# Performance work log

Measured on AMD Instinct MI355X. Metric: run time of the kernel, lower is better.

Reference implementation:

```python
import jax, jax.numpy as jnp
import numpy as np

B, S, D, H = 4, 1024, 512, 8
EPS = 1e-5


def _cx(x):
    # [..., 2] float -> complex
    return jax.lax.complex(x[..., 0], x[..., 1])


def setup_inputs() -> dict:
    key = jax.random.key(0)
    ks = jax.random.split(key, 9)
    f = lambda k, sh: jax.random.normal(k, sh, dtype=jnp.float32)
    inp = {
        "q": f(ks[0], (B, S, D, 2)),
        "k": f(ks[1], (B, S, D, 2)),
        "v": f(ks[2], (B, S, D, 2)),
        "Wq": f(ks[3], (D, D, 2)) * 0.02,
        "bq": f(ks[4], (D, 2)) * 0.02,
        "Wk": f(ks[5], (D, D, 2)) * 0.02,
        "bk": f(ks[6], (D, 2)) * 0.02,
        "Wv": f(ks[7], (D, D, 2)) * 0.02,
        "bv": f(ks[8], (D, 2)) * 0.02,
        "gamma_r": jnp.ones((D,), jnp.float32),
        "beta_r": jnp.zeros((D,), jnp.float32),
        "gamma_i": jnp.ones((D,), jnp.float32),
        "beta_i": jnp.zeros((D,), jnp.float32),
        "n_heads": H,
    }
    return inp


def _layernorm(x, g, b):
    # torch LayerNorm: biased variance, eps inside sqrt
    mu = jnp.mean(x, axis=-1, keepdims=True)
    var = jnp.mean((x - mu) ** 2, axis=-1, keepdims=True)
    return (x - mu) / jnp.sqrt(var + EPS) * g + b


def reference(q, k, v, Wq, bq, Wk, bk, Wv, bv, gamma_r, beta_r, gamma_i, beta_i, n_heads):
    qc, kc, vc = _cx(q), _cx(k), _cx(v)
    # complex linear: x @ W^T + b
    Q = jnp.einsum("bsd,ed->bse", qc, _cx(Wq)) + _cx(bq)
    K = jnp.einsum("bsd,ed->bse", kc, _cx(Wk)) + _cx(bk)
    V = jnp.einsum("bsd,ed->bse", vc, _cx(Wv)) + _cx(bv)
    b, s, d = qc.shape
    dh = d // n_heads
    Qh = Q.reshape(b, s, n_heads, dh)
    Kh = K.reshape(b, s, n_heads, dh)
    Vh = V.reshape(b, s, n_heads, dh)
    # complex scores [b,h,q,k], scaled by sqrt(dh)
    scores = jnp.einsum("bqhd,bkhd->bhqk", Qh, Kh) / jnp.sqrt(jnp.float32(dh))
    # original: softmax over view_as_real dim=-2 == key axis, real & imag independently
    attn = jax.lax.complex(jax.nn.softmax(scores.real, axis=-1),
                           jax.nn.softmax(scores.imag, axis=-1))
    # (dropout is identity in eval mode)
    out = jnp.einsum("bhqk,bkhd->bqhd", attn, Vh).reshape(b, s, d)
    out = out + qc  # residual
    out_r = _layernorm(out.real, gamma_r, beta_r)
    out_i = _layernorm(out.imag, gamma_i, beta_i)
    return jnp.stack([out_r, out_i], axis=-1)  # [B,S,D,2]
```

## Files before the change

### kernel.cpp

```cpp
#include <hip/hip_runtime.h>
#include <math.h>

#define BB  4
#define SS  1024
#define DD  512
#define HH  8
#define DHD 64
#define PL  2097152
#define WPL 262144

constexpr float LN_EPS = 1e-5f;

using half4 = __attribute__((ext_vector_type(4))) _Float16;
using half8 = __attribute__((ext_vector_type(8))) _Float16;
using f32x4 = __attribute__((ext_vector_type(4))) float;

__device__ __forceinline__ half8 negh(half8 a) {
    union { half8 h; unsigned int u[4]; } t;
    t.h = a;
    #pragma unroll
    for (int i = 0; i < 4; ++i) t.u[i] ^= 0x80008000u;
    return t.h;
}
__device__ __forceinline__ half8 ldh64(const unsigned short* p, int row, int col) {
    return *(const half8*)(p + row * 64 + (col ^ ((row & 7) << 3)));
}
#define MFMA16(acc, a, b) acc = __builtin_amdgcn_mfma_f32_16x16x32_f16(a, b, acc, 0, 0, 0)

__global__ __launch_bounds__(256)
void cvt_kernel(const float2* __restrict__ s0, const float2* __restrict__ s1,
                const float2* __restrict__ s2, unsigned short* __restrict__ dst,
                int planeElems) {
    const int z = blockIdx.y;
    const float2* src = z == 0 ? s0 : (z == 1 ? s1 : s2);
    unsigned short* base = dst + (size_t)z * 2 * planeElems;
    const int idx = (blockIdx.x * 256 + threadIdx.x) * 2;
    float4 t = *(const float4*)(src + idx);
    const int m = idx >> 9;
    const int d = idx & 511;
    const int ob = (((m >> 7) << 3) + (d >> 6)) * 8192 + ((m & 127) << 6) + (d & 63);
    union { _Float16 h[2]; unsigned int u; } r, i;
    r.h[0] = (_Float16)t.x; r.h[1] = (_Float16)t.z;
    i.h[0] = (_Float16)t.y; i.h[1] = (_Float16)t.w;
    *(unsigned int*)(base + ob) = r.u;
    *(unsigned int*)(base + planeElems + ob) = i.u;
}

__global__ __launch_bounds__(256, 2)
void proj_kernel(const unsigned short* __restrict__ XP,
                 const unsigned short* __restrict__ WP,
                 const float2* __restrict__ bq, const float2* __restrict__ bk,
                 const float2* __restrict__ bv,
                 unsigned short* __restrict__ QG, unsigned short* __restrict__ KG,
                 unsigned short* __restrict__ VG) {
    const unsigned short* XR = XP + (size_t)blockIdx.z * 2 * PL;
    const unsigned short* XI = XR + PL;
    const unsigned short* WRp = WP + (size_t)blockIdx.z * 2 * WPL;
    const unsigned short* WIp = WRp + WPL;
    const float2* bias; unsigned short* outP;
    if (blockIdx.z == 0)      { bias = bq; outP = QG; }
    else if (blockIdx.z == 1) { bias = bk; outP = KG; }
    else                      { bias = bv; outP = VG; }
    const bool isV = (blockIdx.z == 2);

    __shared__ __align__(16) unsigned short Xs[2][128 * 64];
    __shared__ __align__(16) unsigned short Ws[2][128 * 64];

    const int tid  = threadIdx.x;
    const int w    = tid >> 6;
    const int lane = tid & 63;
    const int quad = lane >> 4;
    const int l15  = lane & 15;
    const int wm   = w >> 1;
    const int we   = w & 1;
    const int m0   = blockIdx.x * 128;
    const int e0   = blockIdx.y * 128;

    const int srow = lane >> 3;
    const int sg   = lane & 7;
    const unsigned short* gplane;
    unsigned short* lb;
    int row0;
    if (w == 0)      { gplane = XR;  row0 = m0; lb = &Xs[0][0]; }
    else if (w == 1) { gplane = XI;  row0 = m0; lb = &Xs[1][0]; }
    else if (w == 2) { gplane = WRp; row0 = e0; lb = &Ws[0][0]; }
    else             { gplane = WIp; row0 = e0; lb = &Ws[1][0]; }
    const unsigned short* gs = gplane + (size_t)row0 * DD + srow * 64 + ((sg ^ srow) << 3);

    f32x4 Sr[4][4], Si[4][4];
    #pragma unroll
    for (int a = 0; a < 4; ++a)
        #pragma unroll
        for (int c = 0; c < 4; ++c) { Sr[a][c] = (f32x4)0.f; Si[a][c] = (f32x4)0.f; }

    for (int s = 0; s < 8; ++s) {
        if (s) __syncthreads();
        const unsigned short* _g = gs + (size_t)s * 8192;
        #pragma unroll
        for (int j = 0; j < 16; ++j)
            __builtin_amdgcn_global_load_lds(
                (const __attribute__((address_space(1))) void*)(_g + j * 512),
                (__attribute__((address_space(3))) void*)(lb + j * 512),
                16, 0, 0);
        __syncthreads();

        #pragma unroll
        for (int kc = 0; kc < 2; ++kc) {
            const int dl = kc * 32 + quad * 8;
            half8 xr[4], xi[4];
            #pragma unroll
            for (int mf = 0; mf < 4; ++mf) {
                const int mr = wm * 64 + mf * 16 + l15;
                xr[mf] = ldh64(Xs[0], mr, dl);
                xi[mf] = ldh64(Xs[1], mr, dl);
            }
            #pragma unroll
            for (int ef = 0; ef < 4; ++ef) {
                const int er = we * 64 + ef * 16 + l15;
                half8 wr  = ldh64(Ws[0], er, dl);
                half8 wi  = ldh64(Ws[1], er, dl);
                half8 wmi = negh(wi);
                #pragma unroll
                for (int mf = 0; mf < 4; ++mf) {
                    MFMA16(Sr[mf][ef], xr[mf], wr);
                    MFMA16(Sr[mf][ef], xi[mf], wmi);
                    MFMA16(Si[mf][ef], xr[mf], wi);
                    MFMA16(Si[mf][ef], xi[mf], wr);
                }
            }
        }
    }

    #pragma unroll
    for (int ef = 0; ef < 4; ++ef) {
        const int eg  = e0 + we * 64 + ef * 16 + l15;
        const int hh  = eg >> 6;
        const int col = eg & 63;
        float2 bb = bias[eg];
        #pragma unroll
        for (int mf = 0; mf < 4; ++mf) {
            #pragma unroll
            for (int reg = 0; reg < 4; ++reg) {
                int m = m0 + wm * 64 + mf * 16 + quad * 4 + reg;
                int bidx = m >> 10;
                int sidx = m & 1023;
                int bh = bidx * HH + hh;
                union { _Float16 h; unsigned short u; } cr, ci;
                cr.h = (_Float16)(Sr[mf][ef][reg] + bb.x);
                ci.h = (_Float16)(Si[mf][ef][reg] + bb.y);
                size_t o = isV ? ((size_t)bh * DHD + col) * SS + sidx
                               : ((size_t)bh * SS + sidx) * DHD + col;
                outP[0 * PL + o] = cr.u;
                outP[1 * PL + o] = ci.u;
            }
        }
    }
}

#define AWID 72
__global__ __launch_bounds__(256, 2)
void attn_kernel(const unsigned short* __restrict__ QG, const unsigned short* __restrict__ KG,
                 const unsigned short* __restrict__ VG,
                 unsigned short* __restrict__ ObR, unsigned short* __restrict__ ObI) {
    __shared__ unsigned short Ks[2][64 * AWID];
    __shared__ unsigned short Vt[2][64 * AWID];
    __shared__ unsigned short Ps[2][64 * AWID];
    __shared__ float lbuf[2][2][64];

    const int n   = blockIdx.x;
    const int bh  = (n & 7) * 4 + (n >> 7);
    const int q0  = ((n >> 3) & 15) * 64;
    const int b   = bh >> 3;
    const int h   = bh & 7;

    const int tid  = threadIdx.x;
    const int w    = tid >> 6;
    const int lane = tid & 63;
    const int quad = lane >> 4;
    const int l15  = lane & 15;
    const int sw   = w & 1;
    const int tw   = w >> 1;

    half8 qfr[2][2], qfi[2][2], qfmi[2][2];
    #pragma unroll
    for (int qt = 0; qt < 2; ++qt)
        #pragma unroll
        for (int kc = 0; kc < 2; ++kc) {
            size_t qa = ((size_t)bh * SS + q0 + sw * 32 + qt * 16 + l15) * DHD + kc * 32 + quad * 8;
            qfr[qt][kc]  = *(const half8*)(QG + qa);
            qfi[qt][kc]  = *(const half8*)(QG + PL + qa);
            qfmi[qt][kc] = negh(qfi[qt][kc]);
        }

    f32x4 acc[2][2][4];
    #pragma unroll
    for (int qt = 0; qt < 2; ++qt)
        #pragma unroll
        for (int dt = 0; dt < 2; ++dt)
            #pragma unroll
            for (int p = 0; p < 4; ++p) acc[qt][dt][p] = (f32x4)0.f;
    float lacc[2][2] = {{0.f, 0.f}, {0.f, 0.f}};

    const int srow = tid >> 3;
    const int sg   = (tid & 7) * 8;

    for (int kt = 0; kt < SS; kt += 64) {
        __syncthreads();
        #pragma unroll
        for (int p = 0; p < 2; ++p)
            #pragma unroll
            for (int it = 0; it < 2; ++it) {
                const int r = it * 32 + srow;
                *(uint4*)&Ks[p][r * AWID + sg] =
                    *(const uint4*)(KG + (size_t)p * PL + ((size_t)bh * SS + kt + r) * DHD + sg);
                *(uint4*)&Vt[p][r * AWID + sg] =
                    *(const uint4*)(VG + (size_t)p * PL + ((size_t)bh * DHD + r) * SS + kt + sg);
            }
        __syncthreads();

        f32x4 Sr[2][2], Si[2][2];
        #pragma unroll
        for (int a = 0; a < 2; ++a)
            #pragma unroll
            for (int c = 0; c < 2; ++c) { Sr[a][c] = (f32x4)0.f; Si[a][c] = (f32x4)0.f; }
        #pragma unroll
        for (int kc = 0; kc < 2; ++kc) {
            #pragma unroll
            for (int kt2 = 0; kt2 < 2; ++kt2) {
                const int krow = tw * 32 + kt2 * 16 + l15;
                half8 akr = *(const half8*)&Ks[0][krow * AWID + kc * 32 + quad * 8];
                half8 aki = *(const half8*)&Ks[1][krow * AWID + kc * 32 + quad * 8];
                #pragma unroll
                for (int qt = 0; qt < 2; ++qt) {
                    MFMA16(Sr[kt2][qt], akr, qfr[qt][kc]);
                    MFMA16(Sr[kt2][qt], aki, qfmi[qt][kc]);
                    MFMA16(Si[kt2][qt], aki, qfr[qt][kc]);
                    MFMA16(Si[kt2][qt], akr, qfi[qt][kc]);
                }
            }
        }

        #pragma unroll
        for (int kt2 = 0; kt2 < 2; ++kt2)
            #pragma unroll
            for (int qt = 0; qt < 2; ++qt) {
                half4 pr, pi;
                float sr_ = 0.f, si_ = 0.f;
                #pragma unroll
                for (int reg = 0; reg < 4; ++reg) {
                    float er = __expf(Sr[kt2][qt][reg] * 0.125f);
                    float ei = __expf(Si[kt2][qt][reg] * 0.125f);
                    pr[reg] = (_Float16)er;
                    pi[reg] = (_Float16)ei;
                    sr_ += (float)pr[reg];
                    si_ += (float)pi[reg];
                }
                lacc[qt][0] += sr_;
                lacc[qt][1] += si_;
                const int qrow = sw * 32 + qt * 16 + l15;
                const int kcol = tw * 32 + kt2 * 16 + quad * 4;
                *(half4*)&Ps[0][qrow * AWID + kcol] = pr;
                *(half4*)&Ps[1][qrow * AWID + kcol] = pi;
            }
        __syncthreads();

        #pragma unroll
        for (int kc = 0; kc < 2; ++kc) {
            half8 ap[2][2];
            #pragma unroll
            for (int qt = 0; qt < 2; ++qt) {
                const int qrow = sw * 32 + qt * 16 + l15;
                ap[qt][0] = *(const half8*)&Ps[0][qrow * AWID + kc * 32 + quad * 8];
                ap[qt][1] = *(const half8*)&Ps[1][qrow * AWID + kc * 32 + quad * 8];
            }
            #pragma unroll
            for (int dt = 0; dt < 2; ++dt) {
                const int drow = tw * 32 + dt * 16 + l15;
                half8 bvr = *(const half8*)&Vt[0][drow * AWID + kc * 32 + quad * 8];
                half8 bvi = *(const half8*)&Vt[1][drow * AWID + kc * 32 + quad * 8];
                #pragma unroll
                for (int qt = 0; qt < 2; ++qt) {
                    MFMA16(acc[qt][dt][0], ap[qt][0], bvr);
                    MFMA16(acc[qt][dt][1], ap[qt][0], bvi);
                    MFMA16(acc[qt][dt][2], ap[qt][1], bvr);
                    MFMA16(acc[qt][dt][3], ap[qt][1], bvi);
                }
            }
        }
    }

    __syncthreads();
    #pragma unroll
    for (int qt = 0; qt < 2; ++qt)
        #pragma unroll
        for (int p = 0; p < 2; ++p) {
            float v = lacc[qt][p];
            v += __shfl_xor(v, 16);
            v += __shfl_xor(v, 32);
            if (lane < 16) lbuf[p][tw][sw * 32 + qt * 16 + lane] = v;
        }
    __syncthreads();

    #pragma unroll
    for (int qt = 0; qt < 2; ++qt)
        #pragma unroll
        for (int reg = 0; reg < 4; ++reg) {
            const int qloc = sw * 32 + qt * 16 + quad * 4 + reg;
            const float ir = 1.f / (lbuf[0][0][qloc] + lbuf[0][1][qloc]);
            const float ii = 1.f / (lbuf[1][0][qloc] + lbuf[1][1][qloc]);
            #pragma unroll
            for (int dt = 0; dt < 2; ++dt) {
                const int d = tw * 32 + dt * 16 + l15;
                union { _Float16 h; unsigned short u; } cr, ci;
                cr.h = (_Float16)(acc[qt][dt][0][reg] * ir - acc[qt][dt][3][reg] * ii);
                ci.h = (_Float16)(acc[qt][dt][1][reg] * ir + acc[qt][dt][2][reg] * ii);
                size_t o = ((size_t)b * SS + q0 + qloc) * DD + h * DHD + d;
                ObR[o] = cr.u;
                ObI[o] = ci.u;
            }
        }
}

__global__ __launch_bounds__(256)
void ln_kernel(const unsigned short* __restrict__ OrP, const unsigned short* __restrict__ OiP,
               const float2* __restrict__ Qin,
               const float* __restrict__ gr, const float* __restrict__ br,
               const float* __restrict__ gi, const float* __restrict__ bi,
               float2* __restrict__ out) {
    const int row = blockIdx.x;
    const int tid = threadIdx.x;
    const size_t base = (size_t)row * DD;
    const int e0 = 2 * tid, e1 = 2 * tid + 1;

    union { unsigned int u; _Float16 h[2]; } tr, ti;
    tr.u = *(const unsigned int*)(OrP + base + e0);
    ti.u = *(const unsigned int*)(OiP + base + e0);
    float2 r0 = Qin[base + e0];
    float2 r1 = Qin[base + e1];
    float xr0 = (float)tr.h[0] + r0.x;
    float xr1 = (float)tr.h[1] + r1.x;
    float xi0 = (float)ti.h[0] + r0.y;
    float xi1 = (float)ti.h[1] + r1.y;

    float sr = xr0 + xr1;
    float si = xi0 + xi1;
    float qr = xr0 * xr0 + xr1 * xr1;
    float qi = xi0 * xi0 + xi1 * xi1;
    #pragma unroll
    for (int off = 32; off > 0; off >>= 1) {
        sr += __shfl_down(sr, off);
        si += __shfl_down(si, off);
        qr += __shfl_down(qr, off);
        qi += __shfl_down(qi, off);
    }
    __shared__ float red[4][4];
    __shared__ float stat[4];
    int lane = tid & 63, wid = tid >> 6;
    if (lane == 0) { red[wid][0] = sr; red[wid][1] = si; red[wid][2] = qr; red[wid][3] = qi; }
    __syncthreads();
    if (tid == 0) {
        sr = red[0][0] + red[1][0] + red[2][0] + red[3][0];
        si = red[0][1] + red[1][1] + red[2][1] + red[3][1];
        qr = red[0][2] + red[1][2] + red[2][2] + red[3][2];
        qi = red[0][3] + red[1][3] + red[2][3] + red[3][3];
        float mur = sr * (1.f / DD), mui = si * (1.f / DD);
        float vr = qr * (1.f / DD) - mur * mur;
        float vi = qi * (1.f / DD) - mui * mui;
        stat[0] = mur; stat[1] = mui;
        stat[2] = rsqrtf(vr + LN_EPS); stat[3] = rsqrtf(vi + LN_EPS);
    }
    __syncthreads();
    float mur = stat[0], mui = stat[1], rsr = stat[2], rsi = stat[3];
    out[base + e0] = make_float2((xr0 - mur) * rsr * gr[e0] + br[e0],
                                 (xi0 - mui) * rsi * gi[e0] + bi[e0]);
    out[base + e1] = make_float2((xr1 - mur) * rsr * gr[e1] + br[e1],
                                 (xi1 - mui) * rsi * gi[e1] + bi[e1]);
}

extern "C" void kernel_launch(void* const* d_in, const int* in_sizes, int n_in,
                              void* d_out, int out_size, void* d_ws, size_t ws_size,
                              hipStream_t stream) {
    const float2* q  = (const float2*)d_in[0];
    const float2* k  = (const float2*)d_in[1];
    const float2* v  = (const float2*)d_in[2];
    const float2* Wq = (const float2*)d_in[3];
    const float2* bq = (const float2*)d_in[4];
    const float2* Wk = (const float2*)d_in[5];
    const float2* bk = (const float2*)d_in[6];
    const float2* Wv = (const float2*)d_in[7];
    const float2* bv = (const float2*)d_in[8];
    const float*  gr = (const float*)d_in[9];
    const float*  br = (const float*)d_in[10];
    const float*  gi = (const float*)d_in[11];
    const float*  bi = (const float*)d_in[12];

    unsigned short* XP  = (unsigned short*)d_ws;
    unsigned short* WP  = XP + (size_t)6 * PL;
    unsigned short* QG  = WP + (size_t)6 * WPL;
    unsigned short* KG  = QG + (size_t)2 * PL;
    unsigned short* VG  = KG + (size_t)2 * PL;
    unsigned short* ObR = VG + (size_t)2 * PL;
    unsigned short* ObI = ObR + (size_t)PL;

    cvt_kernel<<<dim3(4096, 3), 256, 0, stream>>>(q, k, v, XP, PL);
    cvt_kernel<<<dim3(512, 3), 256, 0, stream>>>(Wq, Wk, Wv, WP, WPL);
    proj_kernel<<<dim3(32, 4, 3), 256, 0, stream>>>(XP, WP, bq, bk, bv, QG, KG, VG);
    attn_kernel<<<dim3(512), 256, 0, stream>>>(QG, KG, VG, ObR, ObI);
    ln_kernel<<<dim3(BB * SS), 256, 0, stream>>>(ObR, ObI, q, gr, br, gi, bi, (float2*)d_out);
}
```

Baseline: 207.4 us.

## Load K/V tiles via direct global-to-LDS with XOR swizzle, exp2 softmax, setprio

Replaces register-staged K/V tile loads with global_load_lds direct copies, one wave per plane, into unpadded 64-wide LDS tiles. The tiles use an XOR swizzle so fragment reads avoid bank conflicts, and they are read through ldh64. The softmax exponent now uses exp2f with a folded scale constant, packed cvt_pkrtz conversion, and fp32 partial sums instead of rounded-half sums. MFMA sections are wrapped in s_setprio to favor matrix issue. The loads are still synchronous per tile with no double buffering, and rounding of the softmax sum changes slightly.

```diff
diff --git a/kernel.cpp b/kernel.cpp
--- a/kernel.cpp
+++ b/kernel.cpp
@@ -24,6 +24,11 @@
 }
 __device__ __forceinline__ half8 ldh64(const unsigned short* p, int row, int col) {
     return *(const half8*)(p + row * 64 + (col ^ ((row & 7) << 3)));
+}
+__device__ __forceinline__ unsigned int cvtpk(float a, float b) {
+    union { decltype(__builtin_amdgcn_cvt_pkrtz(0.f, 0.f)) v; unsigned int u; } t;
+    t.v = __builtin_amdgcn_cvt_pkrtz(a, b);
+    return t.u;
 }
 #define MFMA16(acc, a, b) acc = __builtin_amdgcn_mfma_f32_16x16x32_f16(a, b, acc, 0, 0, 0)
 
@@ -162,9 +167,9 @@
 void attn_kernel(const unsigned short* __restrict__ QG, const unsigned short* __restrict__ KG,
                  const unsigned short* __restrict__ VG,
                  unsigned short* __restrict__ ObR, unsigned short* __restrict__ ObI) {
-    __shared__ unsigned short Ks[2][64 * AWID];
-    __shared__ unsigned short Vt[2][64 * AWID];
-    __shared__ unsigned short Ps[2][64 * AWID];
+    __shared__ __align__(16) unsigned short Ks[2][64 * 64];
+    __shared__ __align__(16) unsigned short Vt[2][64 * 64];
+    __shared__ __align__(16) unsigned short Ps[2][64 * AWID];
     __shared__ float lbuf[2][2][64];
 
     const int n   = blockIdx.x;
@@ -181,6 +186,19 @@
     const int sw   = w & 1;
     const int tw   = w >> 1;
 
+    const int srow = lane >> 3;
+    const int sg   = lane & 7;
+    const unsigned short* bp;
+    int jstr, ktmul;
+    unsigned short* ld;
+    if (w < 2) {
+        bp = KG + (size_t)w * PL + (size_t)bh * SS * DHD + srow * DHD + ((sg ^ srow) << 3);
+        jstr = 8 * DHD; ktmul = DHD; ld = &Ks[w][0];
+    } else {
+        bp = VG + (size_t)(w - 2) * PL + (size_t)bh * DHD * SS + srow * SS + ((sg ^ srow) << 3);
+        jstr = 8 * SS; ktmul = 1; ld = &Vt[w - 2][0];
+    }
+
     half8 qfr[2][2], qfi[2][2], qfmi[2][2];
     #pragma unroll
     for (int qt = 0; qt < 2; ++qt)
@@ -201,21 +219,17 @@
             for (int p = 0; p < 4; ++p) acc[qt][dt][p] = (f32x4)0.f;
     float lacc[2][2] = {{0.f, 0.f}, {0.f, 0.f}};
 
-    const int srow = tid >> 3;
-    const int sg   = (tid & 7) * 8;
+    constexpr float EC = 0.18033688011112042f;
 
     for (int kt = 0; kt < SS; kt += 64) {
         __syncthreads();
-        #pragma unroll
-        for (int p = 0; p < 2; ++p)
-            #pragma unroll
-            for (int it = 0; it < 2; ++it) {
-                const int r = it * 32 + srow;
-                *(uint4*)&Ks[p][r * AWID + sg] =
-                    *(const uint4*)(KG + (size_t)p * PL + ((size_t)bh * SS + kt + r) * DHD + sg);
-                *(uint4*)&Vt[p][r * AWID + sg] =
-                    *(const uint4*)(VG + (size_t)p * PL + ((size_t)bh * DHD + r) * SS + kt + sg);
-            }
+        const unsigned short* g = bp + (size_t)kt * ktmul;
+        #pragma unroll
+        for (int j = 0; j < 8; ++j)
+            __builtin_amdgcn_global_load_lds(
+                (const __attribute__((address_space(1))) void*)(g + j * jstr),
+                (__attribute__((address_space(3))) void*)(ld + j * 512),
+                16, 0, 0);
         __syncthreads();
 
         f32x4 Sr[2][2], Si[2][2];
@@ -223,13 +237,15 @@
         for (int a = 0; a < 2; ++a)
             #pragma unroll
             for (int c = 0; c < 2; ++c) { Sr[a][c] = (f32x4)0.f; Si[a][c] = (f32x4)0.f; }
+        __builtin_amdgcn_s_setprio(1);
         #pragma unroll
         for (int kc = 0; kc < 2; ++kc) {
+            const int dl = kc * 32 + quad * 8;
             #pragma unroll
             for (int kt2 = 0; kt2 < 2; ++kt2) {
                 const int krow = tw * 32 + kt2 * 16 + l15;
-                half8 akr = *(const half8*)&Ks[0][krow * AWID + kc * 32 + quad * 8];
-                half8 aki = *(const half8*)&Ks[1][krow * AWID + kc * 32 + quad * 8];
+                half8 akr = ldh64(Ks[0], krow, dl);
+                half8 aki = ldh64(Ks[1], krow, dl);
                 #pragma unroll
                 for (int qt = 0; qt < 2; ++qt) {
                     MFMA16(Sr[kt2][qt], akr, qfr[qt][kc]);
@@ -239,28 +255,25 @@
                 }
             }
         }
+        __builtin_amdgcn_s_setprio(0);
 
         #pragma unroll
         for (int kt2 = 0; kt2 < 2; ++kt2)
             #pragma unroll
             for (int qt = 0; qt < 2; ++qt) {
-                half4 pr, pi;
-                float sr_ = 0.f, si_ = 0.f;
-                #pragma unroll
-                for (int reg = 0; reg < 4; ++reg) {
-                    float er = __expf(Sr[kt2][qt][reg] * 0.125f);
-                    float ei = __expf(Si[kt2][qt][reg] * 0.125f);
-                    pr[reg] = (_Float16)er;
-                    pi[reg] = (_Float16)ei;
-                    sr_ += (float)pr[reg];
-                    si_ += (float)pi[reg];
-                }
-                lacc[qt][0] += sr_;
-                lacc[qt][1] += si_;
+                float er0 = exp2f(Sr[kt2][qt][0] * EC), er1 = exp2f(Sr[kt2][qt][1] * EC);
+                float er2 = exp2f(Sr[kt2][qt][2] * EC), er3 = exp2f(Sr[kt2][qt][3] * EC);
+                float ei0 = exp2f(Si[kt2][qt][0] * EC), ei1 = exp2f(Si[kt2][qt][1] * EC);
+                float ei2 = exp2f(Si[kt2][qt][2] * EC), ei3 = exp2f(Si[kt2][qt][3] * EC);
+                lacc[qt][0] += (er0 + er1) + (er2 + er3);
+                lacc[qt][1] += (ei0 + ei1) + (ei2 + ei3);
                 const int qrow = sw * 32 + qt * 16 + l15;
                 const int kcol = tw * 32 + kt2 * 16 + quad * 4;
-                *(half4*)&Ps[0][qrow * AWID + kcol] = pr;
-                *(half4*)&Ps[1][qrow * AWID + kcol] = pi;
+                uint2 pr, pi;
+                pr.x = cvtpk(er0, er1); pr.y = cvtpk(er2, er3);
+                pi.x = cvtpk(ei0, ei1); pi.y = cvtpk(ei2, ei3);
+                *(uint2*)&Ps[0][qrow * AWID + kcol] = pr;
+                *(uint2*)&Ps[1][qrow * AWID + kcol] = pi;
             }
         __syncthreads();
 
@@ -273,11 +286,12 @@
                 ap[qt][0] = *(const half8*)&Ps[0][qrow * AWID + kc * 32 + quad * 8];
                 ap[qt][1] = *(const half8*)&Ps[1][qrow * AWID + kc * 32 + quad * 8];
             }
+            __builtin_amdgcn_s_setprio(1);
             #pragma unroll
             for (int dt = 0; dt < 2; ++dt) {
                 const int drow = tw * 32 + dt * 16 + l15;
-                half8 bvr = *(const half8*)&Vt[0][drow * AWID + kc * 32 + quad * 8];
-                half8 bvi = *(const half8*)&Vt[1][drow * AWID + kc * 32 + quad * 8];
+                half8 bvr = ldh64(Vt[0], drow, kc * 32 + quad * 8);
+                half8 bvi = ldh64(Vt[1], drow, kc * 32 + quad * 8);
                 #pragma unroll
                 for (int qt = 0; qt < 2; ++qt) {
                     MFMA16(acc[qt][dt][0], ap[qt][0], bvr);
@@ -286,6 +300,7 @@
                     MFMA16(acc[qt][dt][3], ap[qt][1], bvi);
                 }
             }
+            __builtin_amdgcn_s_setprio(0);
         }
     }
 
```

New measurement: 213.5 us. 3.0% more time.
